# Performance work log

Hardware: AMD Instinct MI355X
Metric: run time of the kernel (lower is better)

Reference implementation:

```python
import jax, jax.numpy as jnp
import numpy as np

TAU = 1.0
K = 10
N_NODES = 1048576
N_GRAPHS = 4096


def setup_inputs() -> dict:
    key = jax.random.key(0)
    k1, k2, k3 = jax.random.split(key, 3)
    # per-node scalar logits
    x = jax.random.normal(k1, (N_NODES, 1), dtype=jnp.float32)
    # uniforms for gumbel noise, kept away from {0,1} for log stability
    uniforms = jax.random.uniform(k2, (N_NODES, 3 * K), dtype=jnp.float32,
                                  minval=1e-6, maxval=1.0 - 1e-6)
    # PyG-style ptr: B+1 cumulative offsets, ptr[0]=0, ptr[-1]=N
    cuts = jnp.sort(jax.random.randint(k3, (N_GRAPHS - 1,), 1, N_NODES))
    ptr = jnp.concatenate([jnp.zeros((1,), cuts.dtype), cuts,
                           jnp.full((1,), N_NODES, cuts.dtype)])
    return {"x": x, "uniforms": uniforms, "ptr": ptr}


def reference(x, uniforms, ptr):
    # x: [N, 1] node logits; uniforms: [N, 3k]; ptr: [B+1] segment offsets
    N = x.shape[0]
    B = ptr.shape[0] - 1
    # node i belongs to graph g where ptr[g] <= i < ptr[g+1]
    seg = jnp.searchsorted(ptr, jnp.arange(N), side="right") - 1  # [N]
    gumbel = -jnp.log(-jnp.log(uniforms))                           # [N, 3k]
    noisy = (gumbel + x) / TAU                                      # [N, 3k]
    # segmented softmax over nodes (dim=0 within each graph), per column
    m = jax.ops.segment_max(noisy, seg, num_segments=B)             # [B, 3k]
    e = jnp.exp(noisy - m[seg])                                     # [N, 3k]
    denom = jax.ops.segment_sum(e, seg, num_segments=B)             # [B, 3k]
    probs = e / denom[seg]                                          # [N, 3k]
    # max over the 3k gumbel samples per node
    samples = jnp.max(probs, axis=1)                                # [N]
    return samples[:, None]                                         # [N, 1]
```

## Files before the change

kernel.cpp:

```cpp
#include <hip/hip_runtime.h>

#define NK3 30
#define NKP 15

__device__ __forceinline__ float hw_log2(float a) { return __builtin_amdgcn_logf(a); }
__device__ __forceinline__ float hw_exp2(float a) { return __builtin_amdgcn_exp2f(a); }

__global__ __launch_bounds__(256) void k1_accumulate(
    const float* __restrict__ x, const float* __restrict__ uniforms,
    const int* __restrict__ ptr, float* __restrict__ wsum, int N, int B)
{
    const int wid  = (blockIdx.x << 2) + (threadIdx.x >> 6);
    const int lane = threadIdx.x & 63;
    const int nodesub = lane >> 4;
    const int cp      = lane & 15;
    const bool active = cp < NKP;

    const int base = wid << 7;
    if (base >= N) return;

    int n0 = base + nodesub;
    int lo = 0, hi = B;
    while (hi - lo > 1) { int mid = (lo + hi) >> 1; if (ptr[mid] <= n0) lo = mid; else hi = mid; }
    int seg = lo;
    int ptr_next = ptr[seg + 1];

    float ax = 0.f, ay = 0.f;

    for (int s = 0; s < 32; ++s) {
        const int n = base + (s << 2) + nodesub;
        if (n < N) {
            if (n >= ptr_next) {
                if (active) {
                    atomicAdd(&wsum[seg * NK3 + (cp << 1)    ], ax);
                    atomicAdd(&wsum[seg * NK3 + (cp << 1) + 1], ay);
                }
                ax = 0.f; ay = 0.f;
                do { ++seg; ptr_next = ptr[seg + 1]; } while (n >= ptr_next);
            }
            if (active) {
                const float xe = fmaf(x[n], 1.44269504f, 0.52876637f);
                const float2 u =
                    reinterpret_cast<const float2*>(uniforms + (size_t)n * NK3)[cp];
                const float t0 = hw_log2(-hw_log2(u.x));
                const float t1 = hw_log2(-hw_log2(u.y));
                ax += hw_exp2(xe - t0);
                ay += hw_exp2(xe - t1);
            }
        }
    }
    if (active) {
        atomicAdd(&wsum[seg * NK3 + (cp << 1)    ], ax);
        atomicAdd(&wsum[seg * NK3 + (cp << 1) + 1], ay);
    }
}

__global__ __launch_bounds__(256) void k2_log(float* __restrict__ wsum, int count)
{
    const int i = blockIdx.x * 256 + threadIdx.x;
    if (i < count) wsum[i] = hw_log2(wsum[i]);
}

__global__ __launch_bounds__(256) void k3_output(
    const float* __restrict__ x, const float* __restrict__ uniforms,
    const int* __restrict__ ptr, const float* __restrict__ lw,
    float* __restrict__ out, int N, int B)
{
    const int wid  = (blockIdx.x << 2) + (threadIdx.x >> 6);
    const int lane = threadIdx.x & 63;
    const int base = wid << 8;
    if (base >= N) return;

    const int n0 = base + lane;
    int lo = 0, hi = B;
    while (hi - lo > 1) { int mid = (lo + hi) >> 1; if (ptr[mid] <= n0) lo = mid; else hi = mid; }
    int seg = lo;

    for (int c = 0; c < 4; ++c) {
        const int n = base + (c << 6) + lane;
        if (n >= N) return;
        while (n >= ptr[seg + 1]) ++seg;

        float l[NK3];
#pragma unroll
        for (int j = 0; j < NK3; ++j) l[j] = lw[seg * NK3 + j];

        const float2* row = reinterpret_cast<const float2*>(uniforms + (size_t)n * NK3);
        float mn = 3.0e38f;
#pragma unroll
        for (int k = 0; k < NKP; ++k) {
            const float2 u = row[k];
            const float t0 = hw_log2(-hw_log2(u.x));
            const float t1 = hw_log2(-hw_log2(u.y));
            mn = fminf(mn, fminf(t0 + l[2 * k], t1 + l[2 * k + 1]));
        }
        out[n] = hw_exp2(fmaf(x[n], 1.44269504f, 0.52876637f) - mn);
    }
}

__global__ __launch_bounds__(256) void gnn_fallback(
    const float* __restrict__ x, const float* __restrict__ uniforms,
    const int* __restrict__ ptr, float* __restrict__ out)
{
    const int wave = threadIdx.x >> 6;
    const int lane = threadIdx.x & 63;
    const int g = (blockIdx.x << 2) + wave;
    const int start = ptr[g];
    const int end   = ptr[g + 1];
    if (end <= start) return;

    float acc[NK3];
#pragma unroll
    for (int j = 0; j < NK3; ++j) acc[j] = 0.0f;
    const int iters = (end - start + 63) >> 6;

    for (int it = 0; it < iters; ++it) {
        const int n = start + (it << 6) + lane;
        if (n < end) {
            const float xe = fmaf(x[n], 1.44269504f, 0.52876637f);
            const float2* row = reinterpret_cast<const float2*>(uniforms + (size_t)n * NK3);
#pragma unroll
            for (int k = 0; k < NKP; ++k) {
                float2 u = row[k];
                float t0 = hw_log2(-hw_log2(u.x));
                float t1 = hw_log2(-hw_log2(u.y));
                acc[2 * k]     += hw_exp2(xe - t0);
                acc[2 * k + 1] += hw_exp2(xe - t1);
            }
        }
    }
#pragma unroll
    for (int j = 0; j < NK3; ++j) {
        float v = acc[j];
#pragma unroll
        for (int off = 1; off < 64; off <<= 1) v += __shfl_xor(v, off, 64);
        acc[j] = hw_log2(v);
    }
    for (int it = 0; it < iters; ++it) {
        const int n = start + (it << 6) + lane;
        if (n < end) {
            const float xe = fmaf(x[n], 1.44269504f, 0.52876637f);
            const float2* row = reinterpret_cast<const float2*>(uniforms + (size_t)n * NK3);
            float mn = 3.0e38f;
#pragma unroll
            for (int k = 0; k < NKP; ++k) {
                float2 u = row[k];
                float t0 = hw_log2(-hw_log2(u.x));
                float t1 = hw_log2(-hw_log2(u.y));
                mn = fminf(mn, fminf(t0 + acc[2 * k], t1 + acc[2 * k + 1]));
            }
            out[n] = hw_exp2(xe - mn);
        }
    }
}

extern "C" void kernel_launch(void* const* d_in, const int* in_sizes, int n_in,
                              void* d_out, int out_size, void* d_ws, size_t ws_size,
                              hipStream_t stream) {
    const float* x        = (const float*)d_in[0];
    const float* uniforms = (const float*)d_in[1];
    const int*   ptr      = (const int*)d_in[2];
    float* out = (float*)d_out;

    const int N = in_sizes[0];
    const int B = in_sizes[2] - 1;
    const size_t ws_needed = (size_t)B * NK3 * sizeof(float);

    if (ws_size >= ws_needed && d_ws != nullptr) {
        float* wsum = (float*)d_ws;
        hipMemsetAsync(wsum, 0, ws_needed, stream);

        const int b1 = (N + 511) / 512;
        k1_accumulate<<<b1, 256, 0, stream>>>(x, uniforms, ptr, wsum, N, B);

        const int cnt = B * NK3;
        const int b2 = (cnt + 255) / 256;
        k2_log<<<b2, 256, 0, stream>>>(wsum, cnt);

        const int b3 = (N + 1023) / 1024;
        k3_output<<<b3, 256, 0, stream>>>(x, uniforms, ptr, wsum, out, N, B);
    } else {
        const int blocks = (B + 3) / 4;
        gnn_fallback<<<blocks, 256, 0, stream>>>(x, uniforms, ptr, out);
    }
}
```

Before: 85.25 us.

## Replace log/exp gumbel math with reciprocal form and batch loads in accumulate

Rewrites the softmax algebra so that exp(x+gumbel) = exp(x)/(-log u). This swaps a log2+exp2 per element for one reciprocal, and turns the per-segment log into a reciprocal, so the output becomes exp(x)·max(r·rd) instead of exp(x - min). The accumulate kernel now preloads 8 nodes' uniforms and x values before computing, giving more memory-level parallelism. The reciprocal form drops the max-shift, so exp(x) could overflow or underflow for extreme logits, and precision changes slightly.

```diff
diff --git a/kernel.cpp b/kernel.cpp
--- a/kernel.cpp
+++ b/kernel.cpp
@@ -5,6 +5,8 @@
 
 __device__ __forceinline__ float hw_log2(float a) { return __builtin_amdgcn_logf(a); }
 __device__ __forceinline__ float hw_exp2(float a) { return __builtin_amdgcn_exp2f(a); }
+__device__ __forceinline__ float hw_rcp(float a)  { return __builtin_amdgcn_rcpf(a); }
+
 
 __global__ __launch_bounds__(256) void k1_accumulate(
     const float* __restrict__ x, const float* __restrict__ uniforms,
@@ -15,11 +17,12 @@
     const int nodesub = lane >> 4;
     const int cp      = lane & 15;
     const bool active = cp < NKP;
+    const int cpl     = active ? cp : 0;
 
     const int base = wid << 7;
     if (base >= N) return;
 
-    int n0 = base + nodesub;
+    const int n0 = base + nodesub;
     int lo = 0, hi = B;
     while (hi - lo > 1) { int mid = (lo + hi) >> 1; if (ptr[mid] <= n0) lo = mid; else hi = mid; }
     int seg = lo;
@@ -27,25 +30,33 @@
 
     float ax = 0.f, ay = 0.f;
 
-    for (int s = 0; s < 32; ++s) {
-        const int n = base + (s << 2) + nodesub;
-        if (n < N) {
-            if (n >= ptr_next) {
-                if (active) {
-                    atomicAdd(&wsum[seg * NK3 + (cp << 1)    ], ax);
-                    atomicAdd(&wsum[seg * NK3 + (cp << 1) + 1], ay);
+    for (int s8 = 0; s8 < 4; ++s8) {
+        float2 u[8];
+        float  xv[8];
+#pragma unroll
+        for (int q = 0; q < 8; ++q) {
+            const int n = base + (s8 << 5) + (q << 2) + nodesub;
+            const int nc = (n < N) ? n : (N - 1);
+            u[q]  = reinterpret_cast<const float2*>(uniforms + (size_t)nc * NK3)[cpl];
+            xv[q] = x[nc];
+        }
+#pragma unroll
+        for (int q = 0; q < 8; ++q) {
+            const int n = base + (s8 << 5) + (q << 2) + nodesub;
+            if (n < N) {
+                if (n >= ptr_next) {
+                    if (active) {
+                        atomicAdd(&wsum[seg * NK3 + (cp << 1)    ], ax);
+                        atomicAdd(&wsum[seg * NK3 + (cp << 1) + 1], ay);
+                    }
+                    ax = 0.f; ay = 0.f;
+                    do { ++seg; ptr_next = ptr[seg + 1]; } while (n >= ptr_next);
                 }
-                ax = 0.f; ay = 0.f;
-                do { ++seg; ptr_next = ptr[seg + 1]; } while (n >= ptr_next);
-            }
-            if (active) {
-                const float xe = fmaf(x[n], 1.44269504f, 0.52876637f);
-                const float2 u =
-                    reinterpret_cast<const float2*>(uniforms + (size_t)n * NK3)[cp];
-                const float t0 = hw_log2(-hw_log2(u.x));
-                const float t1 = hw_log2(-hw_log2(u.y));
-                ax += hw_exp2(xe - t0);
-                ay += hw_exp2(xe - t1);
+                const float E  = hw_exp2(xv[q] * 1.44269504f);
+                const float w0 = -hw_log2(u[q].x);
+                const float w1 = -hw_log2(u[q].y);
+                ax = fmaf(E, hw_rcp(w0), ax);
+                ay = fmaf(E, hw_rcp(w1), ay);
             }
         }
     }
@@ -55,15 +66,15 @@
     }
 }
 
-__global__ __launch_bounds__(256) void k2_log(float* __restrict__ wsum, int count)
+__global__ __launch_bounds__(256) void k2_rcp(float* __restrict__ wsum, int count)
 {
     const int i = blockIdx.x * 256 + threadIdx.x;
-    if (i < count) wsum[i] = hw_log2(wsum[i]);
+    if (i < count) wsum[i] = hw_rcp(wsum[i]);
 }
 
 __global__ __launch_bounds__(256) void k3_output(
     const float* __restrict__ x, const float* __restrict__ uniforms,
-    const int* __restrict__ ptr, const float* __restrict__ lw,
+    const int* __restrict__ ptr, const float* __restrict__ rd,
     float* __restrict__ out, int N, int B)
 {
     const int wid  = (blockIdx.x << 2) + (threadIdx.x >> 6);
@@ -83,18 +94,18 @@
 
         float l[NK3];
 #pragma unroll
-        for (int j = 0; j < NK3; ++j) l[j] = lw[seg * NK3 + j];
+        for (int j = 0; j < NK3; ++j) l[j] = rd[seg * NK3 + j];
 
         const float2* row = reinterpret_cast<const float2*>(uniforms + (size_t)n * NK3);
-        float mn = 3.0e38f;
+        float mx = 0.0f;
 #pragma unroll
         for (int k = 0; k < NKP; ++k) {
             const float2 u = row[k];
-            const float t0 = hw_log2(-hw_log2(u.x));
-            const float t1 = hw_log2(-hw_log2(u.y));
-            mn = fminf(mn, fminf(t0 + l[2 * k], t1 + l[2 * k + 1]));
+            const float r0 = hw_rcp(-hw_log2(u.x));
+            const float r1 = hw_rcp(-hw_log2(u.y));
+            mx = fmaxf(mx, fmaxf(r0 * l[2 * k], r1 * l[2 * k + 1]));
         }
-        out[n] = hw_exp2(fmaf(x[n], 1.44269504f, 0.52876637f) - mn);
+        out[n] = hw_exp2(x[n] * 1.44269504f) * mx;
     }
 }
 
@@ -117,15 +128,13 @@
     for (int it = 0; it < iters; ++it) {
         const int n = start + (it << 6) + lane;
         if (n < end) {
-            const float xe = fmaf(x[n], 1.44269504f, 0.52876637f);
+            const float E = hw_exp2(x[n] * 1.44269504f);
             const float2* row = reinterpret_cast<const float2*>(uniforms + (size_t)n * NK3);
 #pragma unroll
             for (int k = 0; k < NKP; ++k) {
                 float2 u = row[k];
-                float t0 = hw_log2(-hw_log2(u.x));
-                float t1 = hw_log2(-hw_log2(u.y));
-                acc[2 * k]     += hw_exp2(xe - t0);
-                acc[2 * k + 1] += hw_exp2(xe - t1);
+                acc[2 * k]     = fmaf(E, hw_rcp(-hw_log2(u.x)), acc[2 * k]);
+                acc[2 * k + 1] = fmaf(E, hw_rcp(-hw_log2(u.y)), acc[2 * k + 1]);
             }
         }
     }
@@ -134,22 +143,21 @@
         float v = acc[j];
 #pragma unroll
         for (int off = 1; off < 64; off <<= 1) v += __shfl_xor(v, off, 64);
-        acc[j] = hw_log2(v);
+        acc[j] = hw_rcp(v);
     }
     for (int it = 0; it < iters; ++it) {
         const int n = start + (it << 6) + lane;
         if (n < end) {
-            const float xe = fmaf(x[n], 1.44269504f, 0.52876637f);
             const float2* row = reinterpret_cast<const float2*>(uniforms + (size_t)n * NK3);
-            float mn = 3.0e38f;
+            float mx = 0.0f;
 #pragma unroll
             for (int k = 0; k < NKP; ++k) {
                 float2 u = row[k];
-                float t0 = hw_log2(-hw_log2(u.x));
-                float t1 = hw_log2(-hw_log2(u.y));
-                mn = fminf(mn, fminf(t0 + acc[2 * k], t1 + acc[2 * k + 1]));
+                const float r0 = hw_rcp(-hw_log2(u.x));
+                const float r1 = hw_rcp(-hw_log2(u.y));
+                mx = fmaxf(mx, fmaxf(r0 * acc[2 * k], r1 * acc[2 * k + 1]));
             }
-            out[n] = hw_exp2(xe - mn);
+            out[n] = hw_exp2(x[n] * 1.44269504f) * mx;
         }
     }
 }
@@ -175,7 +183,7 @@
 
         const int cnt = B * NK3;
         const int b2 = (cnt + 255) / 256;
-        k2_log<<<b2, 256, 0, stream>>>(wsum, cnt);
+        k2_rcp<<<b2, 256, 0, stream>>>(wsum, cnt);
 
         const int b3 = (N + 1023) / 1024;
         k3_output<<<b3, 256, 0, stream>>>(x, uniforms, ptr, wsum, out, N, B);
```

Result: faster. 81.46 us (-4.4%).
